# Kernel optimization log

Hardware: AMD Instinct MI355X
Metric: run time of the kernel (lower is better)

Reference implementation:

```python
import jax, jax.numpy as jnp
import numpy as np

HID = 512; HH = HID // 2; INP = 1; OUT = 1
INH = int(HID * 0.3); EXC = HID - INH            # 153 / 359
N = 3 * HH + 2 * HID + INP                       # 1793 total units
ALM_EXC_START = 3 * HH + HID                      # start of ALM excitatory block
T_CONST = 0.1; SIGMA_REC = 0.01
B, T = 128, 300


def _np_masks():
    rng = np.random.default_rng(0)
    n_zeros = int(np.ceil(0.9 * HH))
    sparse = np.ones((HH, HH), np.float32)
    for c in range(HH):
        sparse[rng.permutation(HH)[:n_zeros], c] = 0.0
    alm2str = np.concatenate([np.ones((HH, EXC), np.float32), np.zeros((HH, INH), np.float32)], 1)
    thal2d1 = np.concatenate([np.ones((HH // 2, HID), np.float32), np.zeros((HH // 2, HID), np.float32)], 0)
    alm2d1 = 1.0 - thal2d1
    iti2d1 = np.concatenate([np.ones((HH // 2, INP), np.float32), np.zeros((HH // 2, INP), np.float32)], 0)
    alm_sign = np.concatenate([np.ones(EXC, np.float32), -np.ones(INH, np.float32)])  # alm2alm_D diagonal
    return sparse, alm2str, thal2d1, alm2d1, iti2d1, alm_sign

_SPARSE, _ALM2STR, _THAL2D1M, _ALM2D1M, _ITI2D1M, _ALMSIGN = [jnp.asarray(a) for a in _np_masks()]


def _clip(w):
    return jnp.clip(w, 1e-10, 1.0)               # F.hardtanh(w, 1e-10, 1)


def _build_W(d12d1_w, d12d2_w, d22d1_w, d22d2_w, d22stn_w, d12thal_w, stn2thal_w,
             thal2alm_w, alm2alm_w, thal2d1_w, thal2d2_w, alm2d1_w, alm2d2_w,
             inp_w_d1, inp_w_d2):
    z_ss = jnp.zeros((HH, HH)); z_sl = jnp.zeros((HH, HID))
    z_ls = jnp.zeros((HID, HH)); z_ll = jnp.zeros((HID, HID))
    z_si = jnp.zeros((HH, INP)); z_li = jnp.zeros((HID, INP))
    # striatal recurrence: sparse_mask * hardtanh(w) @ (-I)
    d12d1 = -(_SPARSE * _clip(d12d1_w)); d12d2 = -(_SPARSE * _clip(d12d2_w))
    d22d1 = -(_SPARSE * _clip(d22d1_w)); d22d2 = -(_SPARSE * _clip(d22d2_w))
    row_d1 = jnp.concatenate([d12d1, d22d1, z_ss, _THAL2D1M * _clip(thal2d1_w),
                              _ALM2D1M * _ALM2STR * _clip(alm2d1_w), _ITI2D1M * _clip(inp_w_d1)], 1)
    row_d2 = jnp.concatenate([d12d2, d22d2, z_ss, _clip(thal2d2_w),
                              _ALM2STR * _clip(alm2d2_w), _clip(inp_w_d2)], 1)
    row_stn = jnp.concatenate([z_ss, _clip(d22stn_w), z_ss, z_sl, z_sl, z_si], 1)
    row_thal = jnp.concatenate([_clip(d12thal_w), z_ls, -_clip(stn2thal_w), z_ll, z_ll, z_li], 1)  # stn2thal @ (-I)
    row_alm = jnp.concatenate([z_ls, z_ls, z_ls, _clip(thal2alm_w),
                               _clip(alm2alm_w) * _ALMSIGN[None, :], z_li], 1)      # alm2alm @ D (Dale)
    row_iti = jnp.zeros((INP, N))
    return jnp.concatenate([row_d1, row_d2, row_stn, row_thal, row_alm, row_iti], 0)


def setup_inputs() -> dict:
    key = jax.random.key(0)
    ks = jax.random.split(key, 24)
    u = lambda k, s: jax.random.uniform(k, s, jnp.float32) * 0.01   # uniform(0, 0.01) init
    return {
        "inp": jax.random.uniform(ks[0], (B, T, INP), jnp.float32),
        "cue_inp": jax.random.uniform(ks[1], (B, T, INP), jnp.float32),
        "inhib_stim": jnp.zeros((B, T, N), jnp.float32),
        "hn": jax.random.uniform(ks[2], (1, B, N), jnp.float32),
        "xn": jax.random.uniform(ks[3], (1, B, N), jnp.float32),
        "noise": jax.random.normal(ks[4], (B, T, N), jnp.float32),
        "d12d1_w": u(ks[5], (HH, HH)), "d12d2_w": u(ks[6], (HH, HH)),
        "d22d1_w": u(ks[7], (HH, HH)), "d22d2_w": u(ks[8], (HH, HH)),
        "d22stn_w": u(ks[9], (HH, HH)), "d12thal_w": u(ks[10], (HID, HH)),
        "stn2thal_w": u(ks[11], (HID, HH)), "thal2alm_w": u(ks[12], (HID, HID)),
        "alm2alm_w": u(ks[13], (HID, HID)), "thal2d1_w": u(ks[14], (HH, HID)),
        "thal2d2_w": u(ks[15], (HH, HID)), "alm2d1_w": u(ks[16], (HH, HID)),
        "alm2d2_w": u(ks[17], (HH, HID)), "inp_w_d1": u(ks[18], (HH, INP)),
        "inp_w_d2": u(ks[19], (HH, INP)), "out_w_alm": u(ks[20], (OUT, EXC)),
    }


def reference(inp, cue_inp, inhib_stim, hn, xn, noise,
              d12d1_w, d12d2_w, d22d1_w, d22d2_w, d22stn_w, d12thal_w, stn2thal_w,
              thal2alm_w, alm2alm_w, thal2d1_w, thal2d2_w, alm2d1_w, alm2d2_w,
              inp_w_d1, inp_w_d2, out_w_alm):
    W = _build_W(d12d1_w, d12d2_w, d22d1_w, d22d2_w, d22stn_w, d12thal_w, stn2thal_w,
                 thal2alm_w, alm2alm_w, thal2d1_w, thal2d2_w, alm2d1_w, alm2d2_w,
                 inp_w_d1, inp_w_d2)
    # tonic current: 0.1 everywhere except ITI units
    tonic = jnp.concatenate([0.1 * jnp.ones(N - INP, jnp.float32), jnp.zeros(INP, jnp.float32)])
    seq = (inhib_stim.swapaxes(0, 1),                 # [T, B, N]
           (inp + cue_inp).swapaxes(0, 1),            # [T, B, INP] -> injected into ITI units
           noise.swapaxes(0, 1))                      # [T, B, N]

    def step(carry, s):
        x, h = carry
        inh_t, iti_t, noise_t = s
        drive = h @ W.T + tonic + inh_t + SIGMA_REC * noise_t
        drive = drive.at[:, N - INP:].add(iti_t)
        x = x + T_CONST * (-x + drive)
        h = jax.nn.relu(x)
        out = h[:, ALM_EXC_START:ALM_EXC_START + EXC] @ out_w_alm.T
        return (x, h), (h, x, out)

    (_, _), (hs, xs, outs) = jax.lax.scan(step, (xn[0], hn[0]), seq)
    return hs.swapaxes(0, 1), xs.swapaxes(0, 1), outs.swapaxes(0, 1)
```

## Files before the change

kernel.cpp:

```cpp
#include <hip/hip_runtime.h>
#include <stdint.h>
#include <string.h>

#define NREAL 1793
#define NPAD  1824
#define NROWP 1808
#define WSTR  1832
#define NBLK  113
#define NGRP  2
#define TSTEPS 300
#define BATCH 128
#define XS_OFF 68851200
#define OUT_OFF 137702400
#define LOFF (16 * WSTR)
#define LOSCALE 4096.0f
#define LOINV  2.44140625e-4f

#define ARR_IDX(g,s)  (((g) * 8 + (s)) * 32)
#define MID_IDX(g)    ((16 + (g)) * 32)
#define FLAG_IDX(g,s) ((18 + (g) * 8 + (s)) * 32)
#define STRIPE_SZ(s)  ((s) == 0 ? 15u : 14u)

typedef _Float16 half_t;
typedef __attribute__((ext_vector_type(8))) _Float16 half8;
typedef __attribute__((ext_vector_type(4))) float f32x4;
typedef __attribute__((ext_vector_type(4))) unsigned int uint4v;

__device__ __forceinline__ float clipw(float w) {
  return fminf(fmaxf(w, 1e-10f), 1.0f);
}

__device__ __forceinline__ void store_h_llc(half_t* p, half_t v) {
  unsigned int u = *(unsigned short*)&v;
  asm volatile("global_store_short %0, %1, off sc0 sc1"
               :: "v"((unsigned long long)(uintptr_t)p), "v"(u)
               : "memory");
}

__global__ __launch_bounds__(256)
void build_w(const float* __restrict__ d12d1, const float* __restrict__ d12d2,
             const float* __restrict__ d22d1, const float* __restrict__ d22d2,
             const float* __restrict__ d22stn, const float* __restrict__ d12thal,
             const float* __restrict__ stn2thal, const float* __restrict__ thal2alm,
             const float* __restrict__ alm2alm, const float* __restrict__ thal2d1,
             const float* __restrict__ thal2d2, const float* __restrict__ alm2d1,
             const float* __restrict__ alm2d2, const float* __restrict__ inpw1,
             const float* __restrict__ inpw2, const unsigned int* __restrict__ mbits,
             half_t* __restrict__ W)
{
  int idx = blockIdx.x * 256 + threadIdx.x;
  if (idx >= NROWP * NPAD) return;
  int i = idx / NPAD, j = idx - (idx / NPAD) * NPAD;
  float v = 0.f;
  if (i < NREAL && j < NREAL) {
    if (i < 256) {
      if (j < 512) {
        int jj = j & 255;
        unsigned bit = (mbits[(i << 3) + (jj >> 5)] >> (jj & 31)) & 1u;
        float wv = (j < 256) ? d12d1[(i << 8) + jj] : d22d1[(i << 8) + jj];
        v = bit ? -clipw(wv) : 0.f;
      } else if (j < 768) {
      } else if (j < 1280) {
        if (i < 128) v = clipw(thal2d1[(i << 9) + (j - 768)]);
      } else if (j < 1792) {
        int jj = j - 1280;
        if (i >= 128 && jj < 359) v = clipw(alm2d1[(i << 9) + jj]);
      } else {
        if (i < 128) v = clipw(inpw1[i]);
      }
    } else if (i < 512) {
      int ii = i - 256;
      if (j < 512) {
        int jj = j & 255;
        unsigned bit = (mbits[(ii << 3) + (jj >> 5)] >> (jj & 31)) & 1u;
        float wv = (j < 256) ? d12d2[(ii << 8) + jj] : d22d2[(ii << 8) + jj];
        v = bit ? -clipw(wv) : 0.f;
      } else if (j < 768) {
      } else if (j < 1280) {
        v = clipw(thal2d2[(ii << 9) + (j - 768)]);
      } else if (j < 1792) {
        int jj = j - 1280;
        if (jj < 359) v = clipw(alm2d2[(ii << 9) + jj]);
      } else {
        v = clipw(inpw2[ii]);
      }
    } else if (i < 768) {
      int ii = i - 512;
      if (j >= 256 && j < 512) v = clipw(d22stn[(ii << 8) + (j - 256)]);
    } else if (i < 1280) {
      int ii = i - 768;
      if (j < 256) v = clipw(d12thal[(ii << 8) + j]);
      else if (j >= 512 && j < 768) v = -clipw(stn2thal[(ii << 8) + (j - 512)]);
    } else if (i < 1792) {
      int ii = i - 1280;
      if (j >= 768 && j < 1280) v = clipw(thal2alm[(ii << 9) + (j - 768)]);
      else if (j >= 1280) {
        int jj = j - 1280;
        v = clipw(alm2alm[(ii << 9) + jj]) * ((jj < 359) ? 1.f : -1.f);
      }
    }
  }
  half_t vh = (half_t)v;
  half_t vl = (half_t)((v - (float)vh) * LOSCALE);
  W[idx] = vh;
  W[(size_t)NROWP * NPAD + idx] = vl;
}

__global__ __launch_bounds__(256)
void init_h(const float* __restrict__ hn, half_t* __restrict__ hbuf)
{
  const size_t P = (size_t)BATCH * NPAD;
  int idx = blockIdx.x * 256 + threadIdx.x;
  if (idx >= BATCH * NPAD) return;
  int b = idx / NPAD, k = idx - b * NPAD;
  float v = (k < NREAL) ? hn[b * NREAL + k] : 0.f;
  half_t vh = (half_t)v;
  half_t vl = (half_t)((v - (float)vh) * LOSCALE);
  hbuf[idx]         = vh;
  hbuf[P + idx]     = vl;
  hbuf[2 * P + idx] = (half_t)0.f;
  hbuf[3 * P + idx] = (half_t)0.f;
}

__global__ __launch_bounds__(256)
void rnn_step_all(const half_t* __restrict__ Wg, half_t* __restrict__ hbuf,
                  unsigned int* __restrict__ cnt,
                  const float* __restrict__ inp, const float* __restrict__ cue,
                  const float* __restrict__ inhib, const float* __restrict__ noise,
                  const float* __restrict__ xn, const float* __restrict__ outw,
                  float* __restrict__ dout)
{
  __shared__ __align__(16) half_t Wl[2 * 16 * WSTR];
  const int tid = threadIdx.x;
  const int bid = blockIdx.x;
  const int g  = bid / NBLK;
  const int nb = bid - g * NBLK;
  const int r0 = nb * 16;
  const int bg = g * 64;
  const size_t P = (size_t)BATCH * NPAD;

  for (int idx = tid; idx < 2 * 16 * (NPAD / 8); idx += 256) {
    int p   = idx / (16 * (NPAD / 8));
    int rem = idx - p * 16 * (NPAD / 8);
    int rr  = rem / (NPAD / 8);
    int cc  = (rem - rr * (NPAD / 8)) * 8;
    *(uint4v*)&Wl[p * LOFF + rr * WSTR + cc] =
        *(const uint4v*)&Wg[(size_t)p * NROWP * NPAD + (size_t)(r0 + rr) * NPAD + cc];
  }
  __syncthreads();

  const int lane = tid & 63;
  const int w    = tid >> 6;
  const int n_i  = lane & 15;
  const int kq   = lane >> 4;
  const int row  = r0 + n_i;
  const bool valid = row < NREAL;
  const int b0 = bg + 16 * w + kq * 4;
  const int bA = bg + 16 * w + n_i;
  const int wl_b = n_i * WSTR + kq * 8;

  int lo0=0,hi0=0,lo1=0,hi1=0,lo2=0,hi2=0;
  if (r0 < 128)       { lo0=0;  hi0=16; lo1=24; hi1=40; lo2=56; hi2=57; }
  else if (r0 < 256)  { lo0=0;  hi0=16; lo1=40; hi1=52; }
  else if (r0 < 512)  { lo0=0;  hi0=16; lo1=24; hi1=52; lo2=56; hi2=57; }
  else if (r0 < 768)  { lo0=8;  hi0=16; }
  else if (r0 < 1280) { lo0=0;  hi0=8;  lo1=16; hi1=24; }
  else if (r0 < 1792) { lo0=24; hi0=56; }

  float xr[4];
  #pragma unroll
  for (int r = 0; r < 4; ++r)
    xr[r] = valid ? xn[(size_t)(b0 + r) * NREAL + row] : 0.f;

  const float wout = (valid && row >= 1280 && row < 1639) ? outw[row - 1280] : 0.f;
  const float tonic = (valid && row < 1792) ? 0.1f : 0.f;
  const bool is_iti = (row == 1792);
  const bool do_out = (r0 >= 1280 && r0 < 1639);

  #pragma unroll 1
  for (int t = 0; t < TSTEPS; ++t) {
    const half_t* hr = hbuf + (size_t)(t & 1) * 2 * P;
    half_t*       hwh = hbuf + (size_t)((t & 1) ^ 1) * 2 * P;
    half_t*       hwl = hwh + P;

    float inh[4], noi[4], itv[4];
    #pragma unroll
    for (int r = 0; r < 4; ++r) {
      int bt = (b0 + r) * TSTEPS + t;
      if (valid) {
        int ei = bt * NREAL + row;
        inh[r] = __builtin_nontemporal_load(&inhib[ei]);
        noi[r] = __builtin_nontemporal_load(&noise[ei]);
      } else { inh[r] = 0.f; noi[r] = 0.f; }
      itv[r] = is_iti ? (inp[bt] + cue[bt]) : 0.f;
    }

    const half8* aph = (const half8*)(hr + (size_t)bA * NPAD + kq * 8);
    const half8* apl = (const half8*)(hr + P + (size_t)bA * NPAD + kq * 8);
    f32x4 acc0 = {0.f, 0.f, 0.f, 0.f};
    f32x4 acc1 = {0.f, 0.f, 0.f, 0.f};
    f32x4 acc2 = {0.f, 0.f, 0.f, 0.f};

#define DO_CHUNK(kc) { \
      half8 avh = aph[(kc) * 4]; \
      half8 avl = apl[(kc) * 4]; \
      half8 bvh = *(const half8*)&Wl[wl_b + (kc) * 32]; \
      half8 bvl = *(const half8*)&Wl[LOFF + wl_b + (kc) * 32]; \
      acc0 = __builtin_amdgcn_mfma_f32_16x16x32_f16(avh, bvh, acc0, 0, 0, 0); \
      acc1 = __builtin_amdgcn_mfma_f32_16x16x32_f16(avh, bvl, acc1, 0, 0, 0); \
      acc2 = __builtin_amdgcn_mfma_f32_16x16x32_f16(avl, bvh, acc2, 0, 0, 0); }

    #pragma unroll 8
    for (int kc = lo0; kc < hi0; ++kc) DO_CHUNK(kc)
    #pragma unroll 8
    for (int kc = lo1; kc < hi1; ++kc) DO_CHUNK(kc)
    #pragma unroll 8
    for (int kc = lo2; kc < hi2; ++kc) DO_CHUNK(kc)
#undef DO_CHUNK

    float op[4];
    #pragma unroll
    for (int r = 0; r < 4; ++r) {
      float drive = acc0[r] + LOINV * (acc1[r] + acc2[r])
                    + tonic + inh[r] + 0.01f * noi[r] + itv[r];
      float xv = xr[r] + 0.1f * (drive - xr[r]);
      float hv = fmaxf(xv, 0.f);
      xr[r] = xv;
      int bt = (b0 + r) * TSTEPS + t;
      if (valid) {
        int ei = bt * NREAL + row;
        __builtin_nontemporal_store(hv, &dout[ei]);
        __builtin_nontemporal_store(xv, &dout[XS_OFF + ei]);
      }
      half_t hh = (half_t)hv;
      half_t hl = (half_t)((hv - (float)hh) * LOSCALE);
      store_h_llc(&hwh[(size_t)(b0 + r) * NPAD + row], hh);
      store_h_llc(&hwl[(size_t)(b0 + r) * NPAD + row], hl);
      op[r] = hv * wout;
    }

    if (do_out) {
      #pragma unroll
      for (int r = 0; r < 4; ++r) {
        float v = op[r];
        v += __shfl_xor(v, 1); v += __shfl_xor(v, 2);
        v += __shfl_xor(v, 4); v += __shfl_xor(v, 8);
        if (n_i == 0) atomicAdd(&dout[OUT_OFF + (b0 + r) * TSTEPS + t], v);
      }
    }

    if (t + 1 < TSTEPS) {
      asm volatile("s_waitcnt vmcnt(0)" ::: "memory");
      __syncthreads();
      if (tid == 0) {
        const int s = nb & 7;
        const unsigned epoch = (unsigned)(t + 1);
        unsigned old = atomicAdd(&cnt[ARR_IDX(g, s)], 1u);
        if (old == epoch * STRIPE_SZ(s) - 1u) {
          unsigned mo = atomicAdd(&cnt[MID_IDX(g)], 1u);
          if (mo == epoch * 8u - 1u) {
            #pragma unroll
            for (int f = 0; f < 8; ++f)
              __hip_atomic_store(&cnt[FLAG_IDX(g, f)], epoch,
                                 __ATOMIC_RELAXED, __HIP_MEMORY_SCOPE_AGENT);
          }
        }
        int spins = 0;
        while (__hip_atomic_load(&cnt[FLAG_IDX(g, s)], __ATOMIC_RELAXED,
                                 __HIP_MEMORY_SCOPE_AGENT) < epoch) {
          if (spins < 2) {
            __builtin_amdgcn_s_sleep(4);
          } else {
            __builtin_amdgcn_s_sleep(16);
          }
          ++spins;
        }
        __builtin_amdgcn_fence(__ATOMIC_ACQUIRE, "agent");
      }
      __syncthreads();
    }
  }
}

static void compute_sparse_mask(uint32_t* mb) {
  uint32_t pool[4];
  uint32_t hc = 0x43b0d7e5u;
  auto hashmix = [&hc](uint32_t value) -> uint32_t {
    value ^= hc; hc *= 0x931e8875u; value *= hc; value ^= value >> 16; return value;
  };
  auto mixf = [](uint32_t x, uint32_t y) -> uint32_t {
    uint32_t r = x * 0xca01f9ddu;
    r -= y * 0x4973f715u;
    r ^= r >> 16;
    return r;
  };
  for (int i = 0; i < 4; ++i) pool[i] = hashmix(0u);
  for (int s = 0; s < 4; ++s)
    for (int d = 0; d < 4; ++d)
      if (s != d) pool[d] = mixf(pool[d], hashmix(pool[s]));
  uint32_t st[8];
  uint32_t hb = 0x8b51f9ddu;
  for (int i = 0; i < 8; ++i) {
    uint32_t dv = pool[i & 3];
    dv ^= hb; hb *= 0x58f38dedu; dv *= hb; dv ^= dv >> 16;
    st[i] = dv;
  }
  uint64_t v64[4];
  for (int i = 0; i < 4; ++i) v64[i] = (uint64_t)st[2 * i] | ((uint64_t)st[2 * i + 1] << 32);
  typedef unsigned __int128 u128;
  const u128 MULT = ((u128)0x2360ed051fc65da4ULL << 64) | 0x4385df649fccf645ULL;
  u128 initstate = ((u128)v64[0] << 64) | v64[1];
  u128 initseq   = ((u128)v64[2] << 64) | v64[3];
  u128 state = 0, inc = (initseq << 1) | 1;
  state = state * MULT + inc;
  state += initstate;
  state = state * MULT + inc;
  bool has32 = false; uint32_t cached = 0;
  auto next64 = [&]() -> uint64_t {
    state = state * MULT + inc;
    uint64_t hi = (uint64_t)(state >> 64), lo = (uint64_t)state;
    unsigned rot = (unsigned)(state >> 122);
    uint64_t x = hi ^ lo;
    return (x >> rot) | (x << ((64 - rot) & 63));
  };
  auto next32 = [&]() -> uint32_t {
    if (has32) { has32 = false; return cached; }
    uint64_t v = next64();
    has32 = true; cached = (uint32_t)(v >> 32);
    return (uint32_t)v;
  };
  auto rinterval = [&](uint32_t mx) -> uint32_t {
    if (mx == 0) return 0;
    uint32_t mask = mx;
    mask |= mask >> 1; mask |= mask >> 2; mask |= mask >> 4;
    mask |= mask >> 8; mask |= mask >> 16;
    uint32_t value;
    do { value = next32() & mask; } while (value > mx);
    return value;
  };
  for (int i = 0; i < 256 * 8; ++i) mb[i] = 0xFFFFFFFFu;
  int perm[256];
  for (int c = 0; c < 256; ++c) {
    for (int i = 0; i < 256; ++i) perm[i] = i;
    for (int i = 255; i >= 1; --i) {
      uint32_t j = rinterval((uint32_t)i);
      int tmp = perm[i]; perm[i] = perm[j]; perm[j] = tmp;
    }
    for (int z = 0; z < 231; ++z)
      mb[perm[z] * 8 + (c >> 5)] &= ~(1u << (c & 31));
  }
}

extern "C" void kernel_launch(void* const* d_in, const int* in_sizes, int n_in,
                              void* d_out, int out_size, void* d_ws, size_t ws_size,
                              hipStream_t stream)
{
  (void)in_sizes; (void)n_in; (void)out_size; (void)ws_size;
  const float* inp   = (const float*)d_in[0];
  const float* cue   = (const float*)d_in[1];
  const float* inhib = (const float*)d_in[2];
  const float* hn    = (const float*)d_in[3];
  const float* xn    = (const float*)d_in[4];
  const float* noise = (const float*)d_in[5];
  const float* outw  = (const float*)d_in[21];
  float* dout = (float*)d_out;

  char* ws = (char*)d_ws;
  const size_t W_BYTES = (size_t)2 * NROWP * NPAD * sizeof(half_t);
  const size_t H_BYTES = (size_t)4 * BATCH * NPAD * sizeof(half_t);
  half_t* W    = (half_t*)ws;
  half_t* hbuf = (half_t*)(ws + W_BYTES);
  unsigned int* mbits = (unsigned int*)(ws + W_BYTES + H_BYTES);
  unsigned int* cnt   = (unsigned int*)(ws + W_BYTES + H_BYTES + 8192);

  static uint32_t hmask[256 * 8];
  compute_sparse_mask(hmask);
  (void)hipMemcpyAsync(mbits, hmask, sizeof(hmask), hipMemcpyHostToDevice, stream);
  (void)hipMemsetAsync(cnt, 0, 8192, stream);
  (void)hipMemsetAsync((char*)d_out + (size_t)OUT_OFF * 4, 0, 38400 * 4, stream);

  build_w<<<(NROWP * NPAD + 255) / 256, 256, 0, stream>>>(
      (const float*)d_in[6],  (const float*)d_in[7],  (const float*)d_in[8],
      (const float*)d_in[9],  (const float*)d_in[10], (const float*)d_in[11],
      (const float*)d_in[12], (const float*)d_in[13], (const float*)d_in[14],
      (const float*)d_in[15], (const float*)d_in[16], (const float*)d_in[17],
      (const float*)d_in[18], (const float*)d_in[19], (const float*)d_in[20],
      mbits, W);
  init_h<<<(BATCH * NPAD + 255) / 256, 256, 0, stream>>>(hn, hbuf);

  void* args[] = {(void*)&W, (void*)&hbuf, (void*)&cnt, (void*)&inp, (void*)&cue,
                  (void*)&inhib, (void*)&noise, (void*)&xn, (void*)&outw, (void*)&dout};
  hipError_t err = hipLaunchCooperativeKernel(reinterpret_cast<void*>(rnn_step_all),
                                              dim3(NGRP * NBLK), dim3(256), args, 0, stream);
  if (err != hipSuccess) {
    rnn_step_all<<<dim3(NGRP * NBLK), dim3(256), 0, stream>>>(
        W, hbuf, cnt, inp, cue, inhib, noise, xn, outw, dout);
  }
}
```

Baseline: 4.808 ms.

## Interleave hi/lo h halves, prefetch next-step inputs, retune barrier spin

The hidden state's high and low fp16 halves are now packed into one 32-bit word. Each step writes a single dword store instead of two short stores, and the A-operand loads read contiguous 16-byte chunks that are split back apart with perm instructions. The inhibition and noise loads for step t+1 are issued before the grid barrier, and the wait only drains older stores (vmcnt(8)), so their latency overlaps the synchronisation. The spin-wait sleep is also shortened. This adds perm ALU work in the inner loop and relies on the vmcnt count correctly covering the h stores before the barrier is signalled.

```diff
diff --git a/kernel.cpp b/kernel.cpp
--- a/kernel.cpp
+++ b/kernel.cpp
@@ -30,10 +30,9 @@
   return fminf(fmaxf(w, 1e-10f), 1.0f);
 }
 
-__device__ __forceinline__ void store_h_llc(half_t* p, half_t v) {
-  unsigned int u = *(unsigned short*)&v;
-  asm volatile("global_store_short %0, %1, off sc0 sc1"
-               :: "v"((unsigned long long)(uintptr_t)p), "v"(u)
+__device__ __forceinline__ void store_pack_llc(uint32_t* p, uint32_t v) {
+  asm volatile("global_store_dword %0, %1, off sc0 sc1"
+               :: "v"((unsigned long long)(uintptr_t)p), "v"(v)
                : "memory");
 }
 
@@ -107,23 +106,23 @@
 }
 
 __global__ __launch_bounds__(256)
-void init_h(const float* __restrict__ hn, half_t* __restrict__ hbuf)
+void init_h(const float* __restrict__ hn, uint32_t* __restrict__ hbuf)
 {
-  const size_t P = (size_t)BATCH * NPAD;
+  const size_t P4 = (size_t)BATCH * NPAD;
   int idx = blockIdx.x * 256 + threadIdx.x;
   if (idx >= BATCH * NPAD) return;
   int b = idx / NPAD, k = idx - b * NPAD;
   float v = (k < NREAL) ? hn[b * NREAL + k] : 0.f;
   half_t vh = (half_t)v;
   half_t vl = (half_t)((v - (float)vh) * LOSCALE);
-  hbuf[idx]         = vh;
-  hbuf[P + idx]     = vl;
-  hbuf[2 * P + idx] = (half_t)0.f;
-  hbuf[3 * P + idx] = (half_t)0.f;
+  uint32_t hp = (uint32_t)(*(unsigned short*)&vh) |
+                ((uint32_t)(*(unsigned short*)&vl) << 16);
+  hbuf[idx]      = hp;
+  hbuf[P4 + idx] = 0u;
 }
 
 __global__ __launch_bounds__(256)
-void rnn_step_all(const half_t* __restrict__ Wg, half_t* __restrict__ hbuf,
+void rnn_step_all(const half_t* __restrict__ Wg, uint32_t* __restrict__ hbuf,
                   unsigned int* __restrict__ cnt,
                   const float* __restrict__ inp, const float* __restrict__ cue,
                   const float* __restrict__ inhib, const float* __restrict__ noise,
@@ -137,17 +136,7 @@
   const int nb = bid - g * NBLK;
   const int r0 = nb * 16;
   const int bg = g * 64;
-  const size_t P = (size_t)BATCH * NPAD;
-
-  for (int idx = tid; idx < 2 * 16 * (NPAD / 8); idx += 256) {
-    int p   = idx / (16 * (NPAD / 8));
-    int rem = idx - p * 16 * (NPAD / 8);
-    int rr  = rem / (NPAD / 8);
-    int cc  = (rem - rr * (NPAD / 8)) * 8;
-    *(uint4v*)&Wl[p * LOFF + rr * WSTR + cc] =
-        *(const uint4v*)&Wg[(size_t)p * NROWP * NPAD + (size_t)(r0 + rr) * NPAD + cc];
-  }
-  __syncthreads();
+  const size_t P4 = (size_t)BATCH * NPAD;
 
   const int lane = tid & 63;
   const int w    = tid >> 6;
@@ -159,6 +148,27 @@
   const int bA = bg + 16 * w + n_i;
   const int wl_b = n_i * WSTR + kq * 8;
 
+  float inh[4], noi[4];
+  #pragma unroll
+  for (int r = 0; r < 4; ++r) {
+    inh[r] = 0.f; noi[r] = 0.f;
+    if (valid) {
+      int ei = ((b0 + r) * TSTEPS) * NREAL + row;
+      inh[r] = __builtin_nontemporal_load(&inhib[ei]);
+      noi[r] = __builtin_nontemporal_load(&noise[ei]);
+    }
+  }
+
+  for (int idx = tid; idx < 2 * 16 * (NPAD / 8); idx += 256) {
+    int p   = idx / (16 * (NPAD / 8));
+    int rem = idx - p * 16 * (NPAD / 8);
+    int rr  = rem / (NPAD / 8);
+    int cc  = (rem - rr * (NPAD / 8)) * 8;
+    *(uint4v*)&Wl[p * LOFF + rr * WSTR + cc] =
+        *(const uint4v*)&Wg[(size_t)p * NROWP * NPAD + (size_t)(r0 + rr) * NPAD + cc];
+  }
+  __syncthreads();
+
   int lo0=0,hi0=0,lo1=0,hi1=0,lo2=0,hi2=0;
   if (r0 < 128)       { lo0=0;  hi0=16; lo1=24; hi1=40; lo2=56; hi2=57; }
   else if (r0 < 256)  { lo0=0;  hi0=16; lo1=40; hi1=52; }
@@ -179,36 +189,40 @@
 
   #pragma unroll 1
   for (int t = 0; t < TSTEPS; ++t) {
-    const half_t* hr = hbuf + (size_t)(t & 1) * 2 * P;
-    half_t*       hwh = hbuf + (size_t)((t & 1) ^ 1) * 2 * P;
-    half_t*       hwl = hwh + P;
-
-    float inh[4], noi[4], itv[4];
+    const uint32_t* hr = hbuf + (size_t)(t & 1) * P4;
+    uint32_t*       hw = hbuf + (size_t)((t & 1) ^ 1) * P4;
+
+    float itv[4];
     #pragma unroll
     for (int r = 0; r < 4; ++r) {
       int bt = (b0 + r) * TSTEPS + t;
-      if (valid) {
-        int ei = bt * NREAL + row;
-        inh[r] = __builtin_nontemporal_load(&inhib[ei]);
-        noi[r] = __builtin_nontemporal_load(&noise[ei]);
-      } else { inh[r] = 0.f; noi[r] = 0.f; }
       itv[r] = is_iti ? (inp[bt] + cue[bt]) : 0.f;
     }
 
-    const half8* aph = (const half8*)(hr + (size_t)bA * NPAD + kq * 8);
-    const half8* apl = (const half8*)(hr + P + (size_t)bA * NPAD + kq * 8);
+    const uint32_t* ap = hr + (size_t)bA * NPAD + kq * 8;
     f32x4 acc0 = {0.f, 0.f, 0.f, 0.f};
     f32x4 acc1 = {0.f, 0.f, 0.f, 0.f};
     f32x4 acc2 = {0.f, 0.f, 0.f, 0.f};
 
 #define DO_CHUNK(kc) { \
-      half8 avh = aph[(kc) * 4]; \
-      half8 avl = apl[(kc) * 4]; \
+      uint4v q0 = *(const uint4v*)(ap + (kc) * 32); \
+      uint4v q1 = *(const uint4v*)(ap + (kc) * 32 + 4); \
+      uint4v uh, ul; \
+      uh.x = __builtin_amdgcn_perm(q0.y, q0.x, 0x05040100u); \
+      uh.y = __builtin_amdgcn_perm(q0.w, q0.z, 0x05040100u); \
+      uh.z = __builtin_amdgcn_perm(q1.y, q1.x, 0x05040100u); \
+      uh.w = __builtin_amdgcn_perm(q1.w, q1.z, 0x05040100u); \
+      ul.x = __builtin_amdgcn_perm(q0.y, q0.x, 0x07060302u); \
+      ul.y = __builtin_amdgcn_perm(q0.w, q0.z, 0x07060302u); \
+      ul.z = __builtin_amdgcn_perm(q1.y, q1.x, 0x07060302u); \
+      ul.w = __builtin_amdgcn_perm(q1.w, q1.z, 0x07060302u); \
+      union { uint4v u; half8 h; } ch, cl; \
+      ch.u = uh; cl.u = ul; \
       half8 bvh = *(const half8*)&Wl[wl_b + (kc) * 32]; \
       half8 bvl = *(const half8*)&Wl[LOFF + wl_b + (kc) * 32]; \
-      acc0 = __builtin_amdgcn_mfma_f32_16x16x32_f16(avh, bvh, acc0, 0, 0, 0); \
-      acc1 = __builtin_amdgcn_mfma_f32_16x16x32_f16(avh, bvl, acc1, 0, 0, 0); \
-      acc2 = __builtin_amdgcn_mfma_f32_16x16x32_f16(avl, bvh, acc2, 0, 0, 0); }
+      acc0 = __builtin_amdgcn_mfma_f32_16x16x32_f16(ch.h, bvh, acc0, 0, 0, 0); \
+      acc1 = __builtin_amdgcn_mfma_f32_16x16x32_f16(ch.h, bvl, acc1, 0, 0, 0); \
+      acc2 = __builtin_amdgcn_mfma_f32_16x16x32_f16(cl.h, bvh, acc2, 0, 0, 0); }
 
     #pragma unroll 8
     for (int kc = lo0; kc < hi0; ++kc) DO_CHUNK(kc)
@@ -234,8 +248,9 @@
       }
       half_t hh = (half_t)hv;
       half_t hl = (half_t)((hv - (float)hh) * LOSCALE);
-      store_h_llc(&hwh[(size_t)(b0 + r) * NPAD + row], hh);
-      store_h_llc(&hwl[(size_t)(b0 + r) * NPAD + row], hl);
+      uint32_t hp = (uint32_t)(*(unsigned short*)&hh) |
+                    ((uint32_t)(*(unsigned short*)&hl) << 16);
+      store_pack_llc(&hw[(size_t)(b0 + r) * NPAD + row], hp);
       op[r] = hv * wout;
     }
 
@@ -250,8 +265,16 @@
     }
 
     if (t + 1 < TSTEPS) {
-      asm volatile("s_waitcnt vmcnt(0)" ::: "memory");
-      __syncthreads();
+      #pragma unroll
+      for (int r = 0; r < 4; ++r) {
+        if (valid) {
+          int ei = ((b0 + r) * TSTEPS + (t + 1)) * NREAL + row;
+          inh[r] = __builtin_nontemporal_load(&inhib[ei]);
+          noi[r] = __builtin_nontemporal_load(&noise[ei]);
+        }
+      }
+      asm volatile("s_waitcnt vmcnt(8)" ::: "memory");
+      __builtin_amdgcn_s_barrier();
       if (tid == 0) {
         const int s = nb & 7;
         const unsigned epoch = (unsigned)(t + 1);
@@ -268,16 +291,16 @@
         int spins = 0;
         while (__hip_atomic_load(&cnt[FLAG_IDX(g, s)], __ATOMIC_RELAXED,
                                  __HIP_MEMORY_SCOPE_AGENT) < epoch) {
-          if (spins < 2) {
-            __builtin_amdgcn_s_sleep(4);
+          if (spins < 4) {
+            __builtin_amdgcn_s_sleep(1);
           } else {
-            __builtin_amdgcn_s_sleep(16);
+            __builtin_amdgcn_s_sleep(8);
           }
           ++spins;
         }
         __builtin_amdgcn_fence(__ATOMIC_ACQUIRE, "agent");
       }
-      __syncthreads();
+      __builtin_amdgcn_s_barrier();
     }
   }
 }
@@ -367,9 +390,9 @@
 
   char* ws = (char*)d_ws;
   const size_t W_BYTES = (size_t)2 * NROWP * NPAD * sizeof(half_t);
-  const size_t H_BYTES = (size_t)4 * BATCH * NPAD * sizeof(half_t);
-  half_t* W    = (half_t*)ws;
-  half_t* hbuf = (half_t*)(ws + W_BYTES);
+  const size_t H_BYTES = (size_t)2 * BATCH * NPAD * 4;
+  half_t*   W    = (half_t*)ws;
+  uint32_t* hbuf = (uint32_t*)(ws + W_BYTES);
   unsigned int* mbits = (unsigned int*)(ws + W_BYTES + H_BYTES);
   unsigned int* cnt   = (unsigned int*)(ws + W_BYTES + H_BYTES + 8192);
 
```

Result: no change. 4.808 ms (-0.0%).
